# Performance work log

Measured on AMD Instinct MI355X. Metric: run time of the kernel, lower is better.

## Reference

```python
import jax, jax.numpy as jnp
import numpy as np

N = 100000   # nodes
E = 3200000  # edges (avg degree 32)
NFEAT = 512
NHID = 8     # forced == 8 by (x_left + x_right) broadcast in the source
NCLASS = 16


def setup_inputs() -> dict:
    key = jax.random.key(0)
    ks = jax.random.split(key, 10)
    x = jax.random.normal(ks[0], (N, NFEAT), dtype=jnp.float32)
    adj_rows = jax.random.randint(ks[1], (E,), 0, N, dtype=jnp.int32)
    adj_cols = jax.random.randint(ks[2], (E,), 0, N, dtype=jnp.int32)
    adj_vals = jax.random.uniform(ks[3], (E,), dtype=jnp.float32)
    s1 = 1.0 / np.sqrt(NFEAT)
    s2 = 1.0 / np.sqrt(NHID)
    W1 = jax.random.normal(ks[4], (NFEAT, NHID), dtype=jnp.float32) * s1
    b1 = jnp.zeros((NHID,), dtype=jnp.float32)
    W2 = jax.random.normal(ks[5], (NHID, NCLASS), dtype=jnp.float32) * s2
    b2 = jnp.zeros((NCLASS,), dtype=jnp.float32)
    V = jax.random.normal(ks[6], (NFEAT, NHID), dtype=jnp.float32) * s1
    gamma = jnp.ones((NHID,), dtype=jnp.float32)
    beta = jnp.zeros((NHID,), dtype=jnp.float32)
    return {"x": x, "adj_rows": adj_rows, "adj_cols": adj_cols, "adj_vals": adj_vals,
            "W1": W1, "b1": b1, "W2": W2, "b2": b2, "V": V, "gamma": gamma, "beta": beta}


def reference(x, adj_rows, adj_cols, adj_vals, W1, b1, W2, b2, V, gamma, beta):
    n = x.shape[0]

    def spmm(support):  # adj @ support, adj in COO
        gathered = adj_vals[:, None] * support[adj_cols]        # [E, F]
        return jax.ops.segment_sum(gathered, adj_rows, num_segments=n)

    # gc1: relu(spmm(adj, x @ W1) + b1)   (dropout off: eval mode)
    x_left = jax.nn.relu(spmm(x @ W1) + b1)                     # [N, 8]

    # BI_Intereaction: FM bi-interaction pooling 0.5*((xV)^2 - (x^2)(V^2))
    xv = x @ V                                                  # [N, 8]
    x2v2 = (x * x) @ (V * V)                                    # [N, 8]
    x_right = jax.nn.relu(0.5 * (xv * xv - x2v2))

    # BatchNorm1d eval mode: running_mean=0, running_var=1 -> affine only
    x_right = gamma * x_right + beta

    h = 0.5 * (x_left + x_right)                                # [N, 8]
    out = spmm(h @ W2) + b2                                     # [N, 16]
    return jax.nn.log_softmax(out, axis=1)
```

## Files before the change

### kernel.cpp

```cpp
#include <hip/hip_runtime.h>
#include <cstdint>
#include <cstddef>


#define NFEAT 512
#define NHID 8
#define NCLASS 16
#define RPB 128
#define NB 512
#define BCAP 4608

__global__ __launch_bounds__(256) void prep_kernel(
    const float* __restrict__ W1, const float* __restrict__ V,
    float* __restrict__ W1T, float* __restrict__ VT, float* __restrict__ VSQT,
    uint4* __restrict__ zero_base, int zero_count16)
{
    int tid = blockIdx.x * 256 + threadIdx.x;
    if (tid < NFEAT * NHID) {
        int k = tid >> 3, j = tid & 7;
        W1T[j * NFEAT + k] = W1[tid];
        float vv = V[tid];
        VT[j * NFEAT + k] = vv;
        VSQT[j * NFEAT + k] = vv * vv;
    }
    int stride = gridDim.x * 256;
    for (int i = tid; i < zero_count16; i += stride)
        zero_base[i] = make_uint4(0u, 0u, 0u, 0u);
}

#define DB_NODES 64
#define DB_CHUNK 32
#define DB_PAD 33

__device__ __forceinline__ void dense_body(
    int node0, int tid,
    const float* __restrict__ x,
    const float* __restrict__ W1T, const float* __restrict__ VT,
    const float* __restrict__ VSQT,
    const float* __restrict__ gamma, const float* __restrict__ beta,
    float* __restrict__ xw1, float* __restrict__ right, int n_nodes,
    float* xs)
{
    const int lane = tid & 63;

    const int j0 = __builtin_amdgcn_readfirstlane(tid >> 6);
    const float* __restrict__ w1a = W1T  + j0 * NFEAT;
    const float* __restrict__ w1b = W1T  + (j0 + 4) * NFEAT;
    const float* __restrict__ va  = VT   + j0 * NFEAT;
    const float* __restrict__ vb  = VT   + (j0 + 4) * NFEAT;
    const float* __restrict__ sa  = VSQT + j0 * NFEAT;
    const float* __restrict__ sb  = VSQT + (j0 + 4) * NFEAT;

    float a1a = 0.f, a1b = 0.f;
    float ava = 0.f, avb = 0.f;
    float a2a = 0.f, a2b = 0.f;

    const int xbase = lane * DB_PAD;

    for (int ch = 0; ch < NFEAT / DB_CHUNK; ++ch) {
        __syncthreads();
#pragma unroll
        for (int t = 0; t < 2; ++t) {
            int i = tid + t * 256;
            int row = i >> 3, col = i & 7;
            int gr = node0 + row;
            if (gr >= n_nodes) gr = n_nodes - 1;
            float4 v = *(const float4*)(x + (size_t)gr * NFEAT + ch * DB_CHUNK + col * 4);
            int b = row * DB_PAD + col * 4;
            xs[b] = v.x; xs[b + 1] = v.y; xs[b + 2] = v.z; xs[b + 3] = v.w;
        }
        __syncthreads();
        const int kof = ch * DB_CHUNK;
#pragma unroll 2
        for (int kk = 0; kk < DB_CHUNK / 4; ++kk) {
            const int kb = kof + kk * 4;
            float x0 = xs[xbase + kk * 4 + 0];
            float x1 = xs[xbase + kk * 4 + 1];
            float x2 = xs[xbase + kk * 4 + 2];
            float x3 = xs[xbase + kk * 4 + 3];
            float q0 = x0 * x0, q1 = x1 * x1, q2 = x2 * x2, q3 = x3 * x3;

            a1a += x0 * w1a[kb] + x1 * w1a[kb + 1] + x2 * w1a[kb + 2] + x3 * w1a[kb + 3];
            a1b += x0 * w1b[kb] + x1 * w1b[kb + 1] + x2 * w1b[kb + 2] + x3 * w1b[kb + 3];
            ava += x0 * va[kb]  + x1 * va[kb + 1]  + x2 * va[kb + 2]  + x3 * va[kb + 3];
            avb += x0 * vb[kb]  + x1 * vb[kb + 1]  + x2 * vb[kb + 2]  + x3 * vb[kb + 3];
            a2a += q0 * sa[kb]  + q1 * sa[kb + 1]  + q2 * sa[kb + 2]  + q3 * sa[kb + 3];
            a2b += q0 * sb[kb]  + q1 * sb[kb + 1]  + q2 * sb[kb + 2]  + q3 * sb[kb + 3];
        }
    }

    int node = node0 + lane;
    if (node < n_nodes) {
        float g0 = gamma[j0], g1 = gamma[j0 + 4];
        float b0 = beta[j0],  b1_ = beta[j0 + 4];
        xw1[node * 8 + j0]     = a1a;
        xw1[node * 8 + j0 + 4] = a1b;
        float ra = fmaxf(0.5f * (ava * ava - a2a), 0.f);
        float rb = fmaxf(0.5f * (avb * avb - a2b), 0.f);
        right[node * 8 + j0]     = 0.5f * (g0 * ra + b0);
        right[node * 8 + j0 + 4] = 0.5f * (g1 * rb + b1_);
    }
}

__global__ __launch_bounds__(256) void dense_kernel(
    const float* __restrict__ x,
    const float* __restrict__ W1T, const float* __restrict__ VT,
    const float* __restrict__ VSQT,
    const float* __restrict__ gamma, const float* __restrict__ beta,
    float* __restrict__ xw1, float* __restrict__ right, int n_nodes)
{
    __shared__ float xs[DB_NODES * DB_PAD];
    dense_body(blockIdx.x * DB_NODES, threadIdx.x, x, W1T, VT, VSQT,
               gamma, beta, xw1, right, n_nodes, xs);
}

__global__ __launch_bounds__(256) void count_dense_kernel(
    const int* __restrict__ rows, int* __restrict__ hist,
    int chunk, int nbins, int e,
    const float* __restrict__ x, const float* __restrict__ W1T,
    const float* __restrict__ VT, const float* __restrict__ VSQT,
    const float* __restrict__ gamma, const float* __restrict__ beta,
    float* __restrict__ xw1, float* __restrict__ right,
    int n_nodes, int dblocks)
{
    __shared__ float xs[DB_NODES * DB_PAD];
    const int bid = blockIdx.x;
    const int tid = threadIdx.x;

    if (bid < dblocks) {
        dense_body(bid * DB_NODES, tid, x, W1T, VT, VSQT,
                   gamma, beta, xw1, right, n_nodes, xs);
        return;
    }

    const int cb = bid - dblocks;
    int* histl = (int*)xs;
    for (int i = tid; i < nbins; i += 256) histl[i] = 0;
    __syncthreads();

    const int base = cb * chunk;
    int lim = e - base; if (lim > chunk) lim = chunk; if (lim < 0) lim = 0;
    const int nq = lim >> 2;
    for (int q = tid; q < nq; q += 256) {
        int4 r4 = *(const int4*)(rows + base + q * 4);
        atomicAdd(&histl[r4.x >> 7], 1);
        atomicAdd(&histl[r4.y >> 7], 1);
        atomicAdd(&histl[r4.z >> 7], 1);
        atomicAdd(&histl[r4.w >> 7], 1);
    }
    const int rem = lim & 3;
    if (tid < rem) atomicAdd(&histl[rows[base + nq * 4 + tid] >> 7], 1);
    __syncthreads();
    for (int i = tid; i < nbins; i += 256)
        hist[(size_t)i * NB + cb] = histl[i];
}

__global__ __launch_bounds__(NB) void scan_kernel(
    const int* __restrict__ hist, int* __restrict__ off,
    int* __restrict__ bintotal)
{
    __shared__ int sa[NB], sb[NB];
    const int bin = blockIdx.x;
    const int tid = threadIdx.x;
    const size_t base = (size_t)bin * NB;

    int h0 = hist[base + tid];
    sa[tid] = h0;
    __syncthreads();
    int* s = sa; int* d = sb;
    for (int o = 1; o < NB; o <<= 1) {
        d[tid] = s[tid] + (tid >= o ? s[tid - o] : 0);
        __syncthreads();
        int* t = s; s = d; d = t;
    }
    off[base + tid] = s[tid] - h0;
    if (tid == NB - 1) bintotal[bin] = s[NB - 1];
}

__global__ __launch_bounds__(256) void place_kernel(
    const int* __restrict__ rows, const int* __restrict__ cols,
    const float* __restrict__ vals, const int* __restrict__ off,
    unsigned long long* __restrict__ binbuf,
    int chunk, int nbins, int e)
{
    __shared__ int cur[2112];
    const int cb = blockIdx.x;
    const int tid = threadIdx.x;

    for (int i = tid; i < nbins; i += 256)
        cur[i] = off[(size_t)i * NB + cb];
    __syncthreads();

    const int base = cb * chunk;
    int lim = e - base; if (lim > chunk) lim = chunk; if (lim < 0) lim = 0;
    const int nq = lim >> 2;
    for (int q = tid; q < nq; q += 256) {
        int i = base + q * 4;
        int4   r4 = *(const int4*)(rows + i);
        int4   c4 = *(const int4*)(cols + i);
        float4 v4 = *(const float4*)(vals + i);
#pragma unroll
        for (int u = 0; u < 4; ++u) {
            int r = (&r4.x)[u], c = (&c4.x)[u];
            float v = (&v4.x)[u];
            int bin = r >> 7;
            int slot = atomicAdd(&cur[bin], 1);
            if (slot < BCAP) {
                unsigned long long ev =
                    ((unsigned long long)__float_as_uint(v) << 32) |
                    ((unsigned)(r & (RPB - 1)) << 17) | (unsigned)(unsigned int)c;
                binbuf[(size_t)bin * BCAP + slot] = ev;
            }
        }
    }
    const int rem = lim & 3;
    if (tid < rem) {
        int i = base + nq * 4 + tid;
        int r = rows[i];
        int bin = r >> 7;
        int slot = atomicAdd(&cur[bin], 1);
        if (slot < BCAP) {
            unsigned long long ev =
                ((unsigned long long)__float_as_uint(vals[i]) << 32) |
                ((unsigned)(r & (RPB - 1)) << 17) | (unsigned)(unsigned int)cols[i];
            binbuf[(size_t)bin * BCAP + slot] = ev;
        }
    }
}

template<int MODE>
__global__ __launch_bounds__(512) void binspmm_kernel(
    const unsigned long long* __restrict__ binbuf,
    const int* __restrict__ bintotal,
    const float* __restrict__ src,
    const float* __restrict__ aux0, const float* __restrict__ aux1,
    float* __restrict__ dst, int n)
{
    __shared__ unsigned long long sorted[BCAP];
    __shared__ int hcnt[RPB];
    __shared__ int hstart[RPB];
    __shared__ int hcur[RPB];
    const int bin = blockIdx.x;
    const int tid = threadIdx.x;

    if (tid < RPB) hcnt[tid] = 0;
    __syncthreads();

    int total = bintotal[bin];
    if (total > BCAP) total = BCAP;
    const unsigned long long* bb = binbuf + (size_t)bin * BCAP;

    for (int s = tid; s < total; s += 512) {
        unsigned long long ev = bb[s];
        atomicAdd(&hcnt[(int)((ev >> 17) & (RPB - 1))], 1);
    }
    __syncthreads();

    if (tid < RPB) hstart[tid] = hcnt[tid];
    __syncthreads();
    for (int o = 1; o < RPB; o <<= 1) {
        int t = 0;
        if (tid < RPB) t = hstart[tid] + (tid >= o ? hstart[tid - o] : 0);
        __syncthreads();
        if (tid < RPB) hstart[tid] = t;
        __syncthreads();
    }
    if (tid < RPB) {
        int ex = hstart[tid] - hcnt[tid];
        hstart[tid] = ex;
        hcur[tid] = ex;
    }
    __syncthreads();

    for (int s = tid; s < total; s += 512) {
        unsigned long long ev = bb[s];
        int rl = (int)((ev >> 17) & (RPB - 1));
        int slot = atomicAdd(&hcur[rl], 1);
        sorted[slot] = ev;
    }
    __syncthreads();

    const int rl = tid >> 2, l = tid & 3;
    const int st = hstart[rl], cn = hcnt[rl];
    float a0 = 0.f, a1 = 0.f, a2 = 0.f, a3 = 0.f;
    float a4 = 0.f, a5 = 0.f, a6 = 0.f, a7 = 0.f;
    for (int i = st + l; i < st + cn; i += 4) {
        unsigned long long ev = sorted[i];
        int col = (int)(ev & 0x1FFFFu);
        float v = __uint_as_float((unsigned)(ev >> 32));
        const float4* sp = (const float4*)(src + (size_t)col * 8);
        float4 lo = sp[0], hi = sp[1];
        a0 += v * lo.x; a1 += v * lo.y; a2 += v * lo.z; a3 += v * lo.w;
        a4 += v * hi.x; a5 += v * hi.y; a6 += v * hi.z; a7 += v * hi.w;
    }
#pragma unroll
    for (int off2 = 1; off2 < 4; off2 <<= 1) {
        a0 += __shfl_xor(a0, off2); a1 += __shfl_xor(a1, off2);
        a2 += __shfl_xor(a2, off2); a3 += __shfl_xor(a3, off2);
        a4 += __shfl_xor(a4, off2); a5 += __shfl_xor(a5, off2);
        a6 += __shfl_xor(a6, off2); a7 += __shfl_xor(a7, off2);
    }

    const int g = bin * RPB + rl;
    if (g >= n) return;

    if (MODE == 0) {
        float s0, s1;
        if (l == 0)      { s0 = a0; s1 = a1; }
        else if (l == 1) { s0 = a2; s1 = a3; }
        else if (l == 2) { s0 = a4; s1 = a5; }
        else             { s0 = a6; s1 = a7; }
        float2 bb2 = ((const float2*)aux0)[l];
        float2 rv  = *(const float2*)(aux1 + (size_t)g * 8 + l * 2);
        float2 w;
        w.x = 0.5f * fmaxf(s0 + bb2.x, 0.f) + rv.x;
        w.y = 0.5f * fmaxf(s1 + bb2.y, 0.f) + rv.y;
        *(float2*)(dst + (size_t)g * 8 + l * 2) = w;
    } else {
        float hv[NHID] = {a0, a1, a2, a3, a4, a5, a6, a7};
        float z[NCLASS];
#pragma unroll
        for (int cc = 0; cc < NCLASS; ++cc) z[cc] = aux1[cc];
#pragma unroll
        for (int j = 0; j < NHID; ++j) {
#pragma unroll
            for (int cc = 0; cc < NCLASS; ++cc)
                z[cc] += hv[j] * aux0[j * NCLASS + cc];
        }
        float m = z[0];
#pragma unroll
        for (int cc = 1; cc < NCLASS; ++cc) m = fmaxf(m, z[cc]);
        float s = 0.f;
#pragma unroll
        for (int cc = 0; cc < NCLASS; ++cc) s += __expf(z[cc] - m);
        float lse = m + __logf(s);
        float o0 = z[4 * l + 0] - lse;
        float o1 = z[4 * l + 1] - lse;
        float o2 = z[4 * l + 2] - lse;
        float o3 = z[4 * l + 3] - lse;
        *(float4*)(dst + (size_t)g * NCLASS + 4 * l) = make_float4(o0, o1, o2, o3);
    }
}

__global__ __launch_bounds__(256) void spmm8_kernel(
    const int* __restrict__ rows, const int* __restrict__ cols,
    const float* __restrict__ vals, const float* __restrict__ src,
    float* __restrict__ acc, int n_edges)
{
    int tid = blockIdx.x * 256 + threadIdx.x;
    int e = tid >> 1;
    if (e >= n_edges) return;
    int hh = tid & 1;
    int r = rows[e], c = cols[e];
    float v = vals[e];
    float4 f = ((const float4*)src)[c * 2 + hh];
    float* d = acc + (size_t)r * NHID + hh * 4;
    unsafeAtomicAdd(d + 0, v * f.x);
    unsafeAtomicAdd(d + 1, v * f.y);
    unsafeAtomicAdd(d + 2, v * f.z);
    unsafeAtomicAdd(d + 3, v * f.w);
}

__global__ __launch_bounds__(256) void mid_kernel(
    const float* __restrict__ acc1, const float* __restrict__ right,
    const float* __restrict__ b1, float* __restrict__ h, int n4)
{
    int i = blockIdx.x * 256 + threadIdx.x;
    if (i >= n4) return;
    float4 a = ((const float4*)acc1)[i];
    float4 r = ((const float4*)right)[i];
    float4 b = ((const float4*)b1)[i & 1];
    float4 o;
    o.x = 0.5f * fmaxf(a.x + b.x, 0.f) + r.x;
    o.y = 0.5f * fmaxf(a.y + b.y, 0.f) + r.y;
    o.z = 0.5f * fmaxf(a.z + b.z, 0.f) + r.z;
    o.w = 0.5f * fmaxf(a.w + b.w, 0.f) + r.w;
    ((float4*)h)[i] = o;
}

__global__ __launch_bounds__(256) void final_kernel(
    const float* __restrict__ acc2, const float* __restrict__ W2,
    const float* __restrict__ b2, float* __restrict__ out, int n_nodes)
{
    int node = blockIdx.x * 256 + threadIdx.x;
    if (node >= n_nodes) return;
    float4 h0 = ((const float4*)acc2)[(size_t)node * 2];
    float4 h1 = ((const float4*)acc2)[(size_t)node * 2 + 1];
    float hv[NHID] = {h0.x, h0.y, h0.z, h0.w, h1.x, h1.y, h1.z, h1.w};
    float z[NCLASS];
#pragma unroll
    for (int c = 0; c < NCLASS; ++c) z[c] = b2[c];
#pragma unroll
    for (int j = 0; j < NHID; ++j) {
#pragma unroll
        for (int c = 0; c < NCLASS; ++c) z[c] += hv[j] * W2[j * NCLASS + c];
    }
    float m = z[0];
#pragma unroll
    for (int c = 1; c < NCLASS; ++c) m = fmaxf(m, z[c]);
    float s = 0.f;
#pragma unroll
    for (int c = 0; c < NCLASS; ++c) s += __expf(z[c] - m);
    float l = m + __logf(s);
    float4* o = (float4*)(out + (size_t)node * NCLASS);
#pragma unroll
    for (int q = 0; q < 4; ++q) {
        float4 tq;
        tq.x = z[4 * q + 0] - l;
        tq.y = z[4 * q + 1] - l;
        tq.z = z[4 * q + 2] - l;
        tq.w = z[4 * q + 3] - l;
        o[q] = tq;
    }
}

extern "C" void kernel_launch(void* const* d_in, const int* in_sizes, int n_in,
                              void* d_out, int out_size, void* d_ws, size_t ws_size,
                              hipStream_t stream)
{
    const float* x     = (const float*)d_in[0];
    const int*   rows  = (const int*)  d_in[1];
    const int*   cols  = (const int*)  d_in[2];
    const float* vals  = (const float*)d_in[3];
    const float* W1    = (const float*)d_in[4];
    const float* b1    = (const float*)d_in[5];
    const float* W2    = (const float*)d_in[6];
    const float* b2    = (const float*)d_in[7];
    const float* V     = (const float*)d_in[8];
    const float* gamma = (const float*)d_in[9];
    const float* beta  = (const float*)d_in[10];

    const int n = in_sizes[0] / NFEAT;
    const int e = in_sizes[1];
    const int nbins = (n + RPB - 1) / RPB;
    const int dblocks = (n + DB_NODES - 1) / DB_NODES;

    float* ws = (float*)d_ws;

    float* xw1   = ws;
    float* right = ws + (size_t)n * 8;
    float* h     = ws + (size_t)n * 16;
    float* W1T   = ws + (size_t)n * 24;
    float* VT    = W1T + NFEAT * NHID;
    float* VSQT  = VT + NFEAT * NHID;
    const size_t fixedf = (size_t)n * 24 + 3 * NFEAT * NHID;
    int* hist     = (int*)(ws + fixedf);
    int* off      = hist + (size_t)nbins * NB;
    int* bintotal = off + (size_t)nbins * NB;
    size_t bb_off = (fixedf + 2ull * nbins * NB + nbins + 1) & ~(size_t)1;
    unsigned long long* binbuf = (unsigned long long*)(ws + bb_off);

    const size_t needf = bb_off + 2ull * nbins * BCAP;
    const bool use_fast =
        (n <= (1 << 17)) && (nbins <= 2112) && (needf * 4 <= ws_size);

    if (use_fast) {
        int chunk = ((e + NB - 1) / NB + 3) & ~3;

        prep_kernel<<<16, 256, 0, stream>>>(
            W1, V, W1T, VT, VSQT, (uint4*)ws, 0);

        count_dense_kernel<<<dblocks + NB, 256, 0, stream>>>(
            rows, hist, chunk, nbins, e,
            x, W1T, VT, VSQT, gamma, beta, xw1, right, n, dblocks);

        scan_kernel<<<nbins, NB, 0, stream>>>(hist, off, bintotal);

        place_kernel<<<NB, 256, 0, stream>>>(
            rows, cols, vals, off, binbuf, chunk, nbins, e);

        binspmm_kernel<0><<<nbins, 512, 0, stream>>>(
            binbuf, bintotal, xw1, b1, right, h, n);

        binspmm_kernel<1><<<nbins, 512, 0, stream>>>(
            binbuf, bintotal, h, W2, b2, (float*)d_out, n);
    } else {
        float* f_acc1  = ws;
        float* f_acc2  = ws + (size_t)n * 8;
        float* f_xw1   = ws + (size_t)n * 16;
        float* f_right = ws + (size_t)n * 24;
        float* f_h     = ws + (size_t)n * 32;
        float* f_W1T   = ws + (size_t)n * 40;
        float* f_VT    = f_W1T + NFEAT * NHID;
        float* f_VSQT  = f_VT + NFEAT * NHID;

        prep_kernel<<<(n * 4 + 255) / 256, 256, 0, stream>>>(
            W1, V, f_W1T, f_VT, f_VSQT, (uint4*)ws, n * 4);

        dense_kernel<<<dblocks, 256, 0, stream>>>(
            x, f_W1T, f_VT, f_VSQT, gamma, beta, f_xw1, f_right, n);

        spmm8_kernel<<<(e * 2 + 255) / 256, 256, 0, stream>>>(rows, cols, vals, f_xw1, f_acc1, e);
        mid_kernel<<<(n * 2 + 255) / 256, 256, 0, stream>>>(f_acc1, f_right, b1, f_h, n * 2);
        spmm8_kernel<<<(e * 2 + 255) / 256, 256, 0, stream>>>(rows, cols, vals, f_h, f_acc2, e);
        final_kernel<<<(n + 255) / 256, 256, 0, stream>>>(f_acc2, W2, b2, (float*)d_out, n);
    }
}
```

Before: 451.0 us.

## Double-buffer dense tile loads, co-schedule dense with place, reuse sorted bins

The dense feature projection now prefetches the next x chunk into registers while computing the current one, using a double-buffered LDS tile so there is one barrier per chunk instead of two. The dense blocks move from the histogram kernel into the placement kernel, and the weight transpose is folded into the histogram kernel, which removes one launch. The first SpMM pass writes its in-LDS sorted edges and per-row offsets to global memory so the second pass can read them directly instead of re-sorting each bin. This costs extra workspace and global writes, and packing dense work with the scatter-heavy place kernel may change how well they overlap.

New measurement: 448.2 us. About the same (-0.6%).

```diff
diff --git a/kernel.cpp b/kernel.cpp
--- a/kernel.cpp
+++ b/kernel.cpp
@@ -10,29 +10,12 @@
 #define NB 512
 #define BCAP 4608
 
-__global__ __launch_bounds__(256) void prep_kernel(
-    const float* __restrict__ W1, const float* __restrict__ V,
-    float* __restrict__ W1T, float* __restrict__ VT, float* __restrict__ VSQT,
-    uint4* __restrict__ zero_base, int zero_count16)
-{
-    int tid = blockIdx.x * 256 + threadIdx.x;
-    if (tid < NFEAT * NHID) {
-        int k = tid >> 3, j = tid & 7;
-        W1T[j * NFEAT + k] = W1[tid];
-        float vv = V[tid];
-        VT[j * NFEAT + k] = vv;
-        VSQT[j * NFEAT + k] = vv * vv;
-    }
-    int stride = gridDim.x * 256;
-    for (int i = tid; i < zero_count16; i += stride)
-        zero_base[i] = make_uint4(0u, 0u, 0u, 0u);
-}
-
 #define DB_NODES 64
 #define DB_CHUNK 32
 #define DB_PAD 33
-
-__device__ __forceinline__ void dense_body(
+#define DB_BUF (DB_NODES * DB_PAD)
+
+__device__ __forceinline__ void dense_body2(
     int node0, int tid,
     const float* __restrict__ x,
     const float* __restrict__ W1T, const float* __restrict__ VT,
@@ -51,33 +34,41 @@
     const float* __restrict__ sa  = VSQT + j0 * NFEAT;
     const float* __restrict__ sb  = VSQT + (j0 + 4) * NFEAT;
 
+    const int row0 = tid >> 3, row1 = row0 + 32;
+    const int col  = tid & 7;
+    int gr0 = node0 + row0; if (gr0 >= n_nodes) gr0 = n_nodes - 1;
+    int gr1 = node0 + row1; if (gr1 >= n_nodes) gr1 = n_nodes - 1;
+    const float4* __restrict__ p0 = (const float4*)(x + (size_t)gr0 * NFEAT) + col;
+    const float4* __restrict__ p1 = (const float4*)(x + (size_t)gr1 * NFEAT) + col;
+    const int b0 = row0 * DB_PAD + col * 4;
+    const int b1 = row1 * DB_PAD + col * 4;
+
     float a1a = 0.f, a1b = 0.f;
     float ava = 0.f, avb = 0.f;
     float a2a = 0.f, a2b = 0.f;
-
     const int xbase = lane * DB_PAD;
 
+    {
+        float4 c0 = p0[0], c1 = p1[0];
+        xs[b0] = c0.x; xs[b0 + 1] = c0.y; xs[b0 + 2] = c0.z; xs[b0 + 3] = c0.w;
+        xs[b1] = c1.x; xs[b1 + 1] = c1.y; xs[b1 + 2] = c1.z; xs[b1 + 3] = c1.w;
+    }
+    __syncthreads();
+
     for (int ch = 0; ch < NFEAT / DB_CHUNK; ++ch) {
-        __syncthreads();
-#pragma unroll
-        for (int t = 0; t < 2; ++t) {
-            int i = tid + t * 256;
-            int row = i >> 3, col = i & 7;
-            int gr = node0 + row;
-            if (gr >= n_nodes) gr = n_nodes - 1;
-            float4 v = *(const float4*)(x + (size_t)gr * NFEAT + ch * DB_CHUNK + col * 4);
-            int b = row * DB_PAD + col * 4;
-            xs[b] = v.x; xs[b + 1] = v.y; xs[b + 2] = v.z; xs[b + 3] = v.w;
-        }
-        __syncthreads();
+        float4 n0, n1;
+        const bool more = (ch + 1) < (NFEAT / DB_CHUNK);
+        if (more) { n0 = p0[(ch + 1) * 8]; n1 = p1[(ch + 1) * 8]; }
+
+        const float* xb = xs + (ch & 1) * DB_BUF + xbase;
         const int kof = ch * DB_CHUNK;
 #pragma unroll 2
         for (int kk = 0; kk < DB_CHUNK / 4; ++kk) {
             const int kb = kof + kk * 4;
-            float x0 = xs[xbase + kk * 4 + 0];
-            float x1 = xs[xbase + kk * 4 + 1];
-            float x2 = xs[xbase + kk * 4 + 2];
-            float x3 = xs[xbase + kk * 4 + 3];
+            float x0 = xb[kk * 4 + 0];
+            float x1 = xb[kk * 4 + 1];
+            float x2 = xb[kk * 4 + 2];
+            float x3 = xb[kk * 4 + 3];
             float q0 = x0 * x0, q1 = x1 * x1, q2 = x2 * x2, q3 = x3 * x3;
 
             a1a += x0 * w1a[kb] + x1 * w1a[kb + 1] + x2 * w1a[kb + 2] + x3 * w1a[kb + 3];
@@ -87,17 +78,24 @@
             a2a += q0 * sa[kb]  + q1 * sa[kb + 1]  + q2 * sa[kb + 2]  + q3 * sa[kb + 3];
             a2b += q0 * sb[kb]  + q1 * sb[kb + 1]  + q2 * sb[kb + 2]  + q3 * sb[kb + 3];
         }
+
+        if (more) {
+            float* d = xs + ((ch + 1) & 1) * DB_BUF;
+            d[b0] = n0.x; d[b0 + 1] = n0.y; d[b0 + 2] = n0.z; d[b0 + 3] = n0.w;
+            d[b1] = n1.x; d[b1 + 1] = n1.y; d[b1 + 2] = n1.z; d[b1 + 3] = n1.w;
+        }
+        __syncthreads();
     }
 
     int node = node0 + lane;
     if (node < n_nodes) {
         float g0 = gamma[j0], g1 = gamma[j0 + 4];
-        float b0 = beta[j0],  b1_ = beta[j0 + 4];
+        float b0_ = beta[j0], b1_ = beta[j0 + 4];
         xw1[node * 8 + j0]     = a1a;
         xw1[node * 8 + j0 + 4] = a1b;
         float ra = fmaxf(0.5f * (ava * ava - a2a), 0.f);
         float rb = fmaxf(0.5f * (avb * avb - a2b), 0.f);
-        right[node * 8 + j0]     = 0.5f * (g0 * ra + b0);
+        right[node * 8 + j0]     = 0.5f * (g0 * ra + b0_);
         right[node * 8 + j0 + 4] = 0.5f * (g1 * rb + b1_);
     }
 }
@@ -109,36 +107,34 @@
     const float* __restrict__ gamma, const float* __restrict__ beta,
     float* __restrict__ xw1, float* __restrict__ right, int n_nodes)
 {
-    __shared__ float xs[DB_NODES * DB_PAD];
-    dense_body(blockIdx.x * DB_NODES, threadIdx.x, x, W1T, VT, VSQT,
-               gamma, beta, xw1, right, n_nodes, xs);
-}
-
-__global__ __launch_bounds__(256) void count_dense_kernel(
+    __shared__ float xs[2 * DB_BUF];
+    dense_body2(blockIdx.x * DB_NODES, threadIdx.x, x, W1T, VT, VSQT,
+                gamma, beta, xw1, right, n_nodes, xs);
+}
+
+__global__ __launch_bounds__(256) void count_prep_kernel(
     const int* __restrict__ rows, int* __restrict__ hist,
     int chunk, int nbins, int e,
-    const float* __restrict__ x, const float* __restrict__ W1T,
-    const float* __restrict__ VT, const float* __restrict__ VSQT,
-    const float* __restrict__ gamma, const float* __restrict__ beta,
-    float* __restrict__ xw1, float* __restrict__ right,
-    int n_nodes, int dblocks)
-{
-    __shared__ float xs[DB_NODES * DB_PAD];
+    const float* __restrict__ W1, const float* __restrict__ V,
+    float* __restrict__ W1T, float* __restrict__ VT, float* __restrict__ VSQT)
+{
+    __shared__ int histl[2112];
     const int bid = blockIdx.x;
     const int tid = threadIdx.x;
 
-    if (bid < dblocks) {
-        dense_body(bid * DB_NODES, tid, x, W1T, VT, VSQT,
-                   gamma, beta, xw1, right, n_nodes, xs);
-        return;
-    }
-
-    const int cb = bid - dblocks;
-    int* histl = (int*)xs;
+    int gt = bid * 256 + tid;
+    if (gt < NFEAT * NHID) {
+        int k = gt >> 3, j = gt & 7;
+        W1T[j * NFEAT + k] = W1[gt];
+        float vv = V[gt];
+        VT[j * NFEAT + k] = vv;
+        VSQT[j * NFEAT + k] = vv * vv;
+    }
+
     for (int i = tid; i < nbins; i += 256) histl[i] = 0;
     __syncthreads();
 
-    const int base = cb * chunk;
+    const int base = bid * chunk;
     int lim = e - base; if (lim > chunk) lim = chunk; if (lim < 0) lim = 0;
     const int nq = lim >> 2;
     for (int q = tid; q < nq; q += 256) {
@@ -152,7 +148,7 @@
     if (tid < rem) atomicAdd(&histl[rows[base + nq * 4 + tid] >> 7], 1);
     __syncthreads();
     for (int i = tid; i < nbins; i += 256)
-        hist[(size_t)i * NB + cb] = histl[i];
+        hist[(size_t)i * NB + bid] = histl[i];
 }
 
 __global__ __launch_bounds__(NB) void scan_kernel(
@@ -177,16 +173,31 @@
     if (tid == NB - 1) bintotal[bin] = s[NB - 1];
 }
 
-__global__ __launch_bounds__(256) void place_kernel(
+__global__ __launch_bounds__(256) void place_dense_kernel(
     const int* __restrict__ rows, const int* __restrict__ cols,
     const float* __restrict__ vals, const int* __restrict__ off,
     unsigned long long* __restrict__ binbuf,
-    int chunk, int nbins, int e)
-{
-    __shared__ int cur[2112];
-    const int cb = blockIdx.x;
+    int chunk, int nbins, int e,
+    const float* __restrict__ x, const float* __restrict__ W1T,
+    const float* __restrict__ VT, const float* __restrict__ VSQT,
+    const float* __restrict__ gamma, const float* __restrict__ beta,
+    float* __restrict__ xw1, float* __restrict__ right,
+    int n_nodes, int dblocks)
+{
+    __shared__ float xs[2 * DB_BUF];
+    const int bid = blockIdx.x;
     const int tid = threadIdx.x;
 
+    if (bid >= NB) {
+        int g = bid - NB;
+        if (g < dblocks)
+            dense_body2(g * DB_NODES, tid, x, W1T, VT, VSQT,
+                        gamma, beta, xw1, right, n_nodes, xs);
+        return;
+    }
+
+    int* cur = (int*)xs;
+    const int cb = bid;
     for (int i = tid; i < nbins; i += 256)
         cur[i] = off[(size_t)i * NB + cb];
     __syncthreads();
@@ -228,12 +239,13 @@
     }
 }
 
-template<int MODE>
-__global__ __launch_bounds__(512) void binspmm_kernel(
+__global__ __launch_bounds__(512) void binspmm0_kernel(
     const unsigned long long* __restrict__ binbuf,
     const int* __restrict__ bintotal,
+    unsigned long long* __restrict__ sortbuf,
+    int* __restrict__ rowstart, int* __restrict__ rowcnt,
     const float* __restrict__ src,
-    const float* __restrict__ aux0, const float* __restrict__ aux1,
+    const float* __restrict__ b1, const float* __restrict__ right,
     float* __restrict__ dst, int n)
 {
     __shared__ unsigned long long sorted[BCAP];
@@ -279,6 +291,13 @@
         sorted[slot] = ev;
     }
     __syncthreads();
+
+    for (int s = tid; s < total; s += 512)
+        sortbuf[(size_t)bin * BCAP + s] = sorted[s];
+    if (tid < RPB) {
+        rowstart[bin * RPB + tid] = hstart[tid];
+        rowcnt[bin * RPB + tid]   = hcnt[tid];
+    }
 
     const int rl = tid >> 2, l = tid & 3;
     const int st = hstart[rl], cn = hcnt[rl];
@@ -304,42 +323,96 @@
     const int g = bin * RPB + rl;
     if (g >= n) return;
 
-    if (MODE == 0) {
-        float s0, s1;
-        if (l == 0)      { s0 = a0; s1 = a1; }
-        else if (l == 1) { s0 = a2; s1 = a3; }
-        else if (l == 2) { s0 = a4; s1 = a5; }
-        else             { s0 = a6; s1 = a7; }
-        float2 bb2 = ((const float2*)aux0)[l];
-        float2 rv  = *(const float2*)(aux1 + (size_t)g * 8 + l * 2);
-        float2 w;
-        w.x = 0.5f * fmaxf(s0 + bb2.x, 0.f) + rv.x;
-        w.y = 0.5f * fmaxf(s1 + bb2.y, 0.f) + rv.y;
-        *(float2*)(dst + (size_t)g * 8 + l * 2) = w;
-    } else {
-        float hv[NHID] = {a0, a1, a2, a3, a4, a5, a6, a7};
-        float z[NCLASS];
-#pragma unroll
-        for (int cc = 0; cc < NCLASS; ++cc) z[cc] = aux1[cc];
-#pragma unroll
-        for (int j = 0; j < NHID; ++j) {
-#pragma unroll
-            for (int cc = 0; cc < NCLASS; ++cc)
-                z[cc] += hv[j] * aux0[j * NCLASS + cc];
-        }
-        float m = z[0];
-#pragma unroll
-        for (int cc = 1; cc < NCLASS; ++cc) m = fmaxf(m, z[cc]);
-        float s = 0.f;
-#pragma unroll
-        for (int cc = 0; cc < NCLASS; ++cc) s += __expf(z[cc] - m);
-        float lse = m + __logf(s);
-        float o0 = z[4 * l + 0] - lse;
-        float o1 = z[4 * l + 1] - lse;
-        float o2 = z[4 * l + 2] - lse;
-        float o3 = z[4 * l + 3] - lse;
-        *(float4*)(dst + (size_t)g * NCLASS + 4 * l) = make_float4(o0, o1, o2, o3);
-    }
+    float s0, s1;
+    if (l == 0)      { s0 = a0; s1 = a1; }
+    else if (l == 1) { s0 = a2; s1 = a3; }
+    else if (l == 2) { s0 = a4; s1 = a5; }
+    else             { s0 = a6; s1 = a7; }
+    float2 bb2 = ((const float2*)b1)[l];
+    float2 rv  = *(const float2*)(right + (size_t)g * 8 + l * 2);
+    float2 w;
+    w.x = 0.5f * fmaxf(s0 + bb2.x, 0.f) + rv.x;
+    w.y = 0.5f * fmaxf(s1 + bb2.y, 0.f) + rv.y;
+    *(float2*)(dst + (size_t)g * 8 + l * 2) = w;
+}
+
+__global__ __launch_bounds__(512) void walk1_kernel(
+    const unsigned long long* __restrict__ sortbuf,
+    const int* __restrict__ rowstart, const int* __restrict__ rowcnt,
+    const float* __restrict__ src,
+    const float* __restrict__ W2, const float* __restrict__ b2,
+    float* __restrict__ out, int n)
+{
+    const int bin = blockIdx.x;
+    const int tid = threadIdx.x;
+    const int rl = tid >> 2, l = tid & 3;
+
+    const int st = rowstart[bin * RPB + rl];
+    const int cn = rowcnt[bin * RPB + rl];
+    const unsigned long long* bb = sortbuf + (size_t)bin * BCAP;
+
+    float a0 = 0.f, a1 = 0.f, a2 = 0.f, a3 = 0.f;
+    float a4 = 0.f, a5 = 0.f, a6 = 0.f, a7 = 0.f;
+    for (int i = st + l; i < st + cn; i += 4) {
+        unsigned long long ev = bb[i];
+        int col = (int)(ev & 0x1FFFFu);
+        float v = __uint_as_float((unsigned)(ev >> 32));
+        const float4* sp = (const float4*)(src + (size_t)col * 8);
+        float4 lo = sp[0], hi = sp[1];
+        a0 += v * lo.x; a1 += v * lo.y; a2 += v * lo.z; a3 += v * lo.w;
+        a4 += v * hi.x; a5 += v * hi.y; a6 += v * hi.z; a7 += v * hi.w;
+    }
+#pragma unroll
+    for (int off2 = 1; off2 < 4; off2 <<= 1) {
+        a0 += __shfl_xor(a0, off2); a1 += __shfl_xor(a1, off2);
+        a2 += __shfl_xor(a2, off2); a3 += __shfl_xor(a3, off2);
+        a4 += __shfl_xor(a4, off2); a5 += __shfl_xor(a5, off2);
+        a6 += __shfl_xor(a6, off2); a7 += __shfl_xor(a7, off2);
+    }
+
+    const int g = bin * RPB + rl;
+    if (g >= n) return;
+
+    float hv[NHID] = {a0, a1, a2, a3, a4, a5, a6, a7};
+    float z[NCLASS];
+#pragma unroll
+    for (int cc = 0; cc < NCLASS; ++cc) z[cc] = b2[cc];
+#pragma unroll
+    for (int j = 0; j < NHID; ++j) {
+#pragma unroll
+        for (int cc = 0; cc < NCLASS; ++cc)
+            z[cc] += hv[j] * W2[j * NCLASS + cc];
+    }
+    float m = z[0];
+#pragma unroll
+    for (int cc = 1; cc < NCLASS; ++cc) m = fmaxf(m, z[cc]);
+    float s = 0.f;
+#pragma unroll
+    for (int cc = 0; cc < NCLASS; ++cc) s += __expf(z[cc] - m);
+    float lse = m + __logf(s);
+    float o0 = z[4 * l + 0] - lse;
+    float o1 = z[4 * l + 1] - lse;
+    float o2 = z[4 * l + 2] - lse;
+    float o3 = z[4 * l + 3] - lse;
+    *(float4*)(out + (size_t)g * NCLASS + 4 * l) = make_float4(o0, o1, o2, o3);
+}
+
+__global__ __launch_bounds__(256) void prep_kernel(
+    const float* __restrict__ W1, const float* __restrict__ V,
+    float* __restrict__ W1T, float* __restrict__ VT, float* __restrict__ VSQT,
+    uint4* __restrict__ zero_base, int zero_count16)
+{
+    int tid = blockIdx.x * 256 + threadIdx.x;
+    if (tid < NFEAT * NHID) {
+        int k = tid >> 3, j = tid & 7;
+        W1T[j * NFEAT + k] = W1[tid];
+        float vv = V[tid];
+        VT[j * NFEAT + k] = vv;
+        VSQT[j * NFEAT + k] = vv * vv;
+    }
+    int stride = gridDim.x * 256;
+    for (int i = tid; i < zero_count16; i += stride)
+        zero_base[i] = make_uint4(0u, 0u, 0u, 0u);
 }
 
 __global__ __launch_bounds__(256) void spmm8_kernel(
@@ -447,33 +520,35 @@
     int* hist     = (int*)(ws + fixedf);
     int* off      = hist + (size_t)nbins * NB;
     int* bintotal = off + (size_t)nbins * NB;
-    size_t bb_off = (fixedf + 2ull * nbins * NB + nbins + 1) & ~(size_t)1;
-    unsigned long long* binbuf = (unsigned long long*)(ws + bb_off);
-
-    const size_t needf = bb_off + 2ull * nbins * BCAP;
+    int* rowstart = bintotal + nbins;
+    int* rowcnt   = rowstart + (size_t)nbins * RPB;
+    size_t bb_off = (fixedf + 2ull * nbins * NB + nbins + 2ull * nbins * RPB + 1)
+                    & ~(size_t)1;
+    unsigned long long* binbuf  = (unsigned long long*)(ws + bb_off);
+    unsigned long long* sortbuf = binbuf + (size_t)nbins * BCAP;
+
+    const size_t needf = bb_off + 4ull * nbins * BCAP;
     const bool use_fast =
         (n <= (1 << 17)) && (nbins <= 2112) && (needf * 4 <= ws_size);
 
     if (use_fast) {
         int chunk = ((e + NB - 1) / NB + 3) & ~3;
 
-        prep_kernel<<<16, 256, 0, stream>>>(
-            W1, V, W1T, VT, VSQT, (uint4*)ws, 0);
-
-        count_dense_kernel<<<dblocks + NB, 256, 0, stream>>>(
-            rows, hist, chunk, nbins, e,
+        count_prep_kernel<<<NB, 256, 0, stream>>>(
+            rows, hist, chunk, nbins, e, W1, V, W1T, VT, VSQT);
+
+        scan_kernel<<<nbins, NB, 0, stream>>>(hist, off, bintotal);
+
+        place_dense_kernel<<<NB + dblocks, 256, 0, stream>>>(
+            rows, cols, vals, off, binbuf, chunk, nbins, e,
             x, W1T, VT, VSQT, gamma, beta, xw1, right, n, dblocks);
 
-        scan_kernel<<<nbins, NB, 0, stream>>>(hist, off, bintotal);
-
-        place_kernel<<<NB, 256, 0, stream>>>(
-            rows, cols, vals, off, binbuf, chunk, nbins, e);
-
-        binspmm_kernel<0><<<nbins, 512, 0, stream>>>(
-            binbuf, bintotal, xw1, b1, right, h, n);
-
-        binspmm_kernel<1><<<nbins, 512, 0, stream>>>(
-            binbuf, bintotal, h, W2, b2, (float*)d_out, n);
+        binspmm0_kernel<<<nbins, 512, 0, stream>>>(
+            binbuf, bintotal, sortbuf, rowstart, rowcnt,
+            xw1, b1, right, h, n);
+
+        walk1_kernel<<<nbins, 512, 0, stream>>>(
+            sortbuf, rowstart, rowcnt, h, W2, b2, (float*)d_out, n);
     } else {
         float* f_acc1  = ws;
         float* f_acc2  = ws + (size_t)n * 8;
```
